# Performance work log

Measured on AMD Instinct MI355X. Metric: run time of the kernel, lower is better.

## Reference

```python
import jax, jax.numpy as jnp
import numpy as np

B, T, R, E, H = 64, 512, 256, 512, 1024

def setup_inputs() -> dict:
    key = jax.random.key(0)
    ks = jax.random.split(key, 7)
    s = lambda d: 1.0 / np.sqrt(d)
    return {
        "x": jax.random.normal(ks[0], (B, T, R), jnp.float32),
        "W_emb": jax.random.normal(ks[1], (E, R), jnp.float32) * s(R),
        "b_emb": jax.random.normal(ks[2], (E,), jnp.float32) * s(R),
        "W_ih": jax.random.normal(ks[3], (4 * H, E), jnp.float32) * s(H),
        "W_hh": jax.random.normal(ks[4], (4 * H, H), jnp.float32) * s(H),
        "b_ih": jax.random.normal(ks[5], (4 * H,), jnp.float32) * s(H),
        "b_hh": jax.random.normal(ks[6], (4 * H,), jnp.float32) * s(H),
    }

def reference(x, W_emb, b_emb, W_ih, W_hh, b_ih, b_hh):
    # Per-timestep Linear embedding, batched over time (same math as the loop)
    xe = jnp.einsum('btr,er->bte', x, W_emb) + b_emb            # [B,T,E]
    # Input contribution to all gates, precomputed for every step
    gx = jnp.einsum('bte,ge->btg', xe, W_ih) + (b_ih + b_hh)    # [B,T,4H]

    def step(carry, gx_t):
        h, c = carry
        gates = gx_t + h @ W_hh.T                               # [B,4H]
        i, f, g, o = jnp.split(gates, 4, axis=-1)
        i = jax.nn.sigmoid(i)
        f = jax.nn.sigmoid(f)
        g = jnp.tanh(g)
        o = jax.nn.sigmoid(o)
        c_new = f * c + i * g
        h_new = o * jnp.tanh(c_new)
        return (h_new, c_new), h_new

    h0 = jnp.zeros((x.shape[0], H), x.dtype)
    c0 = jnp.zeros((x.shape[0], H), x.dtype)
    (h_t, c_t), ys = jax.lax.scan(step, (h0, c0), jnp.swapaxes(gx, 0, 1))
    outputs = jnp.swapaxes(ys, 0, 1)                            # [B,T,H]
    return outputs, h_t, c_t
```

## Files before the change

### kernel.cpp

```cpp
#include <hip/hip_runtime.h>
#include <stdint.h>

typedef __attribute__((ext_vector_type(8))) short short8;
typedef __attribute__((ext_vector_type(4))) float f32x4;
typedef __attribute__((ext_vector_type(4))) unsigned short ushort4v;
typedef unsigned long long u64;

__device__ inline unsigned short f2bf(float x) {
  union { float f; unsigned u; } v; v.f = x;
  unsigned r = (v.u + 0x7FFFu + ((v.u >> 16) & 1u)) >> 16;
  return (unsigned short)r;
}
__device__ inline float bf2f(unsigned short b) {
  union { unsigned u; float f; } v; v.u = ((unsigned)b) << 16;
  return v.f;
}
__device__ inline float fsig(float x) { return 1.f / (1.f + __expf(-x)); }

__device__ inline void gload_lds16(const void* g, void* l) {
  __builtin_amdgcn_global_load_lds(
      (const __attribute__((address_space(1))) unsigned int*)g,
      (__attribute__((address_space(3))) unsigned int*)l, 16, 0, 0);
}

__global__ void k_convert(const float* __restrict__ src, unsigned short* __restrict__ dst, int n4) {
  int i = blockIdx.x * blockDim.x + threadIdx.x;
  if (i < n4) {
    f32x4 v = *(const f32x4*)(src + (size_t)i * 4);
    ushort4v r;
    r.x = f2bf(v.x); r.y = f2bf(v.y); r.z = f2bf(v.z); r.w = f2bf(v.w);
    *(ushort4v*)(dst + (size_t)i * 4) = r;
  }
}

__global__ void k_temb(const float* __restrict__ We, unsigned short* __restrict__ WT) {
  int o = blockIdx.x * blockDim.x + threadIdx.x;
  int r = o >> 9, e = o & 511;
  WT[o] = f2bf(We[e * 256 + r]);
}

__global__ void k_bcomb(const float* __restrict__ Wih, const float* __restrict__ b_emb,
                        const float* __restrict__ b_ih, const float* __restrict__ b_hh,
                        float* __restrict__ out) {
  int g = blockIdx.x * blockDim.x + threadIdx.x;
  const float* row = Wih + (size_t)g * 512;
  float s = 0.f;
  for (int e = 0; e < 512; ++e) s += row[e] * b_emb[e];
  out[g] = s + b_ih[g] + b_hh[g];
}

__global__ void k_init(unsigned short* __restrict__ h0, unsigned short* __restrict__ flags,
                       float* __restrict__ zerob) {
  int i = blockIdx.x * blockDim.x + threadIdx.x;
  h0[i] = 0;
  if (i < 256) { flags[i] = 0; zerob[i] = 0.f; }
}

template <int MODE>
__global__ __launch_bounds__(256) void k_gemm_bt(
    const unsigned short* __restrict__ A,
    const unsigned short* __restrict__ Bm,
    const float* __restrict__ bias,
    unsigned short* __restrict__ C,
    int M, int N, int K) {
  __shared__ unsigned short As[128 * 32];
  __shared__ unsigned short Bs[128 * 32];
  const int tid = threadIdx.x;

  int bidx = blockIdx.x, bidy = blockIdx.y;
  if (MODE == 1) {
    int bid = blockIdx.y * gridDim.x + blockIdx.x;
    int cpx = (gridDim.x * gridDim.y) >> 3;
    int swz = (bid & 7) * cpx + (bid >> 3);
    bidy = swz / gridDim.x;
    bidx = swz % gridDim.x;
  }
  const int m0 = bidy * 128, n0 = bidx * 128;
  const int lane = tid & 63, w = tid >> 6;
  const int wm = (w >> 1) * 64, wn = (w & 1) * 64;

  f32x4 acc[4][4] = {};

  const int ar0 = tid >> 2;
  const int ak = (tid & 3) * 8;
  const unsigned short* Ag0 = A + (size_t)(m0 + ar0) * K + ak;
  const unsigned short* Ag1 = A + (size_t)(m0 + 64 + ar0) * K + ak;
  const unsigned short* Bg0 = Bm + (size_t)(n0 + ar0) * K + ak;
  const unsigned short* Bg1 = Bm + (size_t)(n0 + 64 + ar0) * K + ak;
  unsigned short* Al = As + tid * 8;
  unsigned short* Bl = Bs + tid * 8;

  const int lr = lane & 15, lk = (lane >> 4) * 8;

  for (int k0 = 0; k0 < K; k0 += 32) {
    gload_lds16(Ag0 + k0, Al);
    gload_lds16(Ag1 + k0, Al + 2048);
    gload_lds16(Bg0 + k0, Bl);
    gload_lds16(Bg1 + k0, Bl + 2048);
    __syncthreads();
    short8 a[4], b[4];
#pragma unroll
    for (int i = 0; i < 4; i++) a[i] = *(const short8*)&As[(wm + i * 16 + lr) * 32 + lk];
#pragma unroll
    for (int j = 0; j < 4; j++) b[j] = *(const short8*)&Bs[(wn + j * 16 + lr) * 32 + lk];
#pragma unroll
    for (int i = 0; i < 4; i++)
#pragma unroll
      for (int j = 0; j < 4; j++)
        acc[i][j] = __builtin_amdgcn_mfma_f32_16x16x32_bf16(a[i], b[j], acc[i][j], 0, 0, 0);
    __syncthreads();
  }

  const int lq = (lane >> 4) * 4;
#pragma unroll
  for (int j = 0; j < 4; j++) {
    int col = n0 + wn + j * 16 + lr;
    float bv = bias[col];
#pragma unroll
    for (int i = 0; i < 4; i++) {
      int rowb = m0 + wm + i * 16 + lq;
#pragma unroll
      for (int r = 0; r < 4; r++) {
        int row = rowb + r;
        float v = acc[i][j][r] + bv;
        if (MODE == 1) {
          int t = row & 511, bglob = row >> 9;
          int gg = bglob >> 4, bb = bglob & 15;
          int s = col >> 10, cc = col & 1023;
          int gtb = cc >> 4, cl = cc & 15;
          int wv = cl >> 2, qq = cl & 3;
          size_t idx = (size_t)t * 262144 + (size_t)gg * 65536 + (size_t)gtb * 1024
                     + (size_t)((wv * 64 + bb * 4 + qq) * 4 + s);
          C[idx] = f2bf(v);
        } else {
          C[(size_t)row * (size_t)N + col] = f2bf(v);
        }
      }
    }
  }
}

#define R32(F) F(0) F(1) F(2) F(3) F(4) F(5) F(6) F(7) \
               F(8) F(9) F(10) F(11) F(12) F(13) F(14) F(15) \
               F(16) F(17) F(18) F(19) F(20) F(21) F(22) F(23) \
               F(24) F(25) F(26) F(27) F(28) F(29) F(30) F(31)
#define WDECL(i) short8 w##i;
#define WLOAD(i) asm volatile("global_load_dwordx4 %0, %1, off offset:%c2" \
                              : "=v"(w##i) : "v"(wbase), "i"((i) * 64));
#define MFH(i, ACC) { \
    short8 a_ = *(const short8*)(HsB + lB + (i) * 1024); \
    ACC = __builtin_amdgcn_mfma_f32_16x16x32_bf16(a_, w##i, ACC, 0, 0, 0); }
#define MF2(i, ACC) { \
    union { u64 d[2]; short8 s; } u_; \
    u_.d[0] = __hip_atomic_load((const u64*)(hrow2 + (i) * 32), __ATOMIC_RELAXED, __HIP_MEMORY_SCOPE_AGENT); \
    u_.d[1] = __hip_atomic_load((const u64*)(hrow2 + (i) * 32 + 4), __ATOMIC_RELAXED, __HIP_MEMORY_SCOPE_AGENT); \
    ACC = __builtin_amdgcn_mfma_f32_16x16x32_bf16(u_.s, w##i, ACC, 0, 0, 0); }

template <int RING>
__global__ __launch_bounds__(256, 1) void k_persist(
    const unsigned short* __restrict__ gx3,
    const unsigned short* __restrict__ Whh,
    unsigned short* __restrict__ hring,
    unsigned short* __restrict__ flags,
    float* __restrict__ out,
    float* __restrict__ hout,
    float* __restrict__ cout) {
  __shared__ unsigned short Hs[16384];
  __shared__ float Gs[4][16 * 17 + 4];

  const int tid = threadIdx.x;
  const int g = blockIdx.x & 3, gt = blockIdx.x >> 2;
  const int lane = tid & 63, w = tid >> 6;
  const int lr = lane & 15, hi = lane >> 4;

  const int grow = (lr >> 2) * 1024 + gt * 16 + w * 4 + (lr & 3);
  const unsigned short* wbase = Whh + (size_t)grow * 1024 + hi * 8;
  R32(WDECL)
  R32(WLOAD)
  asm volatile("s_waitcnt vmcnt(0)" ::: "memory");
  __builtin_amdgcn_sched_barrier(0);

  const int cb = lane >> 2, cq = lane & 3;
  const int col = gt * 16 + w * 4 + cq;
  const int brow = g * 16 + cb;
  float c_reg = 0.f;

  const u64* gbase = (const u64*)gx3 + (size_t)g * 16384 + (size_t)gt * 256;
  u64 gv = gbase[tid];

  const char* HsB = (const char*)Hs;
  const int lB = hi * 256 + lr * 16;

  const u64* fpw = (const u64*)flags + g * 16 + w * 4 + (lane & 3);

  for (int t = 0; t < 512; ++t) {
    f32x4 ac0 = {}, ac1 = {}, ac2 = {}, ac3 = {};
    if (RING == 2) {
      if (w == 0) {
        const u64* fp = (const u64*)flags + g * 16 + lane;
        for (;;) {
          bool ok = true;
          if (lane < 16) {
            u64 f = __hip_atomic_load(fp, __ATOMIC_RELAXED, __HIP_MEMORY_SCOPE_AGENT);
            ok = ((int)(f & 0xFFFF) >= t) && ((int)((f >> 16) & 0xFFFF) >= t) &&
                 ((int)((f >> 32) & 0xFFFF) >= t) && ((int)(f >> 48) >= t);
          }
          if (__all(ok)) break;
        }
      }
      __syncthreads();
      __builtin_amdgcn_sched_barrier(0);
      const unsigned short* hrow2 = hring + (size_t)(t & 1) * 65536
                                  + (size_t)(g * 16 + lr) * 1024 + hi * 8;
      MF2(0, ac0)  MF2(1, ac1)  MF2(2, ac2)  MF2(3, ac3)
      MF2(4, ac0)  MF2(5, ac1)  MF2(6, ac2)  MF2(7, ac3)
      MF2(8, ac0)  MF2(9, ac1)  MF2(10, ac2) MF2(11, ac3)
      MF2(12, ac0) MF2(13, ac1) MF2(14, ac2) MF2(15, ac3)
      MF2(16, ac0) MF2(17, ac1) MF2(18, ac2) MF2(19, ac3)
      MF2(20, ac0) MF2(21, ac1) MF2(22, ac2) MF2(23, ac3)
      MF2(24, ac0) MF2(25, ac1) MF2(26, ac2) MF2(27, ac3)
      MF2(28, ac0) MF2(29, ac1) MF2(30, ac2) MF2(31, ac3)
    } else {
      for (;;) {
        u64 f = __hip_atomic_load(fpw, __ATOMIC_RELAXED, __HIP_MEMORY_SCOPE_AGENT);
        bool ok = ((int)(f & 0xFFFF) >= t) && ((int)((f >> 16) & 0xFFFF) >= t) &&
                  ((int)((f >> 32) & 0xFFFF) >= t) && ((int)(f >> 48) >= t);
        if (__all(ok)) break;
      }
      __builtin_amdgcn_sched_barrier(0);
      const unsigned short* hsrc = hring + (size_t)t * 65536 + (size_t)g * 16384;
#pragma unroll
      for (int i = 0; i < 8; ++i) {
        int ch = w * 512 + i * 64;
        gload_lds16(hsrc + ((size_t)ch + lane) * 8, Hs + (size_t)ch * 8);
      }
      asm volatile("s_waitcnt vmcnt(0)" ::: "memory");
      __builtin_amdgcn_sched_barrier(0);
      __syncthreads();
      MFH(0, ac0)  MFH(1, ac1)  MFH(2, ac2)  MFH(3, ac3)
      MFH(4, ac0)  MFH(5, ac1)  MFH(6, ac2)  MFH(7, ac3)
      MFH(8, ac0)  MFH(9, ac1)  MFH(10, ac2) MFH(11, ac3)
      MFH(12, ac0) MFH(13, ac1) MFH(14, ac2) MFH(15, ac3)
      MFH(16, ac0) MFH(17, ac1) MFH(18, ac2) MFH(19, ac3)
      MFH(20, ac0) MFH(21, ac1) MFH(22, ac2) MFH(23, ac3)
      MFH(24, ac0) MFH(25, ac1) MFH(26, ac2) MFH(27, ac3)
      MFH(28, ac0) MFH(29, ac1) MFH(30, ac2) MFH(31, ac3)
    }
    f32x4 accs = (ac0 + ac1) + (ac2 + ac3);

#pragma unroll
    for (int r = 0; r < 4; ++r)
      Gs[w][(hi * 4 + r) * 17 + lr] = accs[r];
    asm volatile("s_waitcnt lgkmcnt(0)" ::: "memory");
    __builtin_amdgcn_sched_barrier(0);

    float gi = Gs[w][cb * 17 + 0 + cq]  + bf2f((unsigned short)(gv));
    float gf = Gs[w][cb * 17 + 4 + cq]  + bf2f((unsigned short)(gv >> 16));
    float gg = Gs[w][cb * 17 + 8 + cq]  + bf2f((unsigned short)(gv >> 32));
    float go = Gs[w][cb * 17 + 12 + cq] + bf2f((unsigned short)(gv >> 48));
    float i_ = fsig(gi);
    float f_ = fsig(gf);
    float g_ = tanhf(gg);
    float o_ = fsig(go);
    float cn = f_ * c_reg + i_ * g_;
    float hn = o_ * tanhf(cn);
    c_reg = cn;

    if (t == 511) {
      __builtin_nontemporal_store(hn, &out[((size_t)brow * 512 + t) * 1024 + col]);
      hout[(size_t)brow * 1024 + col] = hn;
      cout[(size_t)brow * 1024 + col] = cn;
    } else {
      unsigned hu = f2bf(hn);
      unsigned v0 = __shfl(hu, (lane & ~3) + 0);
      unsigned v1 = __shfl(hu, (lane & ~3) + 1);
      unsigned v2 = __shfl(hu, (lane & ~3) + 2);
      unsigned v3 = __shfl(hu, (lane & ~3) + 3);
      if ((lane & 3) == 0) {
        u64 pack = (u64)(v0 & 0xFFFF) | ((u64)(v1 & 0xFFFF) << 16)
                 | ((u64)(v2 & 0xFFFF) << 32) | ((u64)(v3 & 0xFFFF) << 48);
        u64* hp;
        if (RING == 2) {
          hp = (u64*)(hring + (size_t)((t + 1) & 1) * 65536
                      + (size_t)brow * 1024 + gt * 16 + w * 4);
        } else {
          size_t e = (size_t)(gt * 2 + (w >> 1)) * 128 + (size_t)cb * 8 + (size_t)(w & 1) * 4;
          hp = (u64*)(hring + (size_t)(t + 1) * 65536 + (size_t)g * 16384 + e);
        }
        __hip_atomic_store(hp, pack, __ATOMIC_RELAXED, __HIP_MEMORY_SCOPE_AGENT);
      }
      __syncthreads();
      if (tid == 0)
        __hip_atomic_store(&flags[g * 64 + gt], (unsigned short)(t + 1),
                           __ATOMIC_RELAXED, __HIP_MEMORY_SCOPE_AGENT);
      __builtin_nontemporal_store(hn, &out[((size_t)brow * 512 + t) * 1024 + col]);
      gv = gbase[(size_t)(t + 1) * 65536 + tid];
    }
  }
}
#undef MF2
#undef MFH
#undef WLOAD
#undef WDECL
#undef R32

extern "C" void kernel_launch(void* const* d_in, const int* in_sizes, int n_in,
                              void* d_out, int out_size, void* d_ws, size_t ws_size,
                              hipStream_t stream) {
  const float* x = (const float*)d_in[0];
  const float* W_emb = (const float*)d_in[1];
  const float* b_emb = (const float*)d_in[2];
  const float* W_ih = (const float*)d_in[3];
  const float* W_hh = (const float*)d_in[4];
  const float* b_ih = (const float*)d_in[5];
  const float* b_hh = (const float*)d_in[6];

  char* ws = (char*)d_ws;
  unsigned short* x_bf    = (unsigned short*)(ws + 0);
  unsigned short* WembT   = (unsigned short*)(ws + 16777216);
  unsigned short* Wih_bf  = (unsigned short*)(ws + 17039360);
  unsigned short* Whh_bf  = (unsigned short*)(ws + 21233664);
  float* b_comb           = (float*)(ws + 29622272);
  float* zerob            = (float*)(ws + 29638656);
  unsigned short* Wcomb   = (unsigned short*)(ws + 29639680);
  unsigned short* gx3     = (unsigned short*)(ws + 63193088);
  unsigned short* flags   = (unsigned short*)(ws + 331628544);
  unsigned short* hring   = (unsigned short*)(ws + 331632640);

  const size_t need_ring = 331632640ull + 512ull * 131072ull;
  const bool big = (ws_size >= need_ring);

  float* out = (float*)d_out;
  float* hout = out + (size_t)64 * 512 * 1024;
  float* cout = hout + 65536;

  k_convert<<<8192, 256, 0, stream>>>(x, x_bf, 2097152);
  k_convert<<<2048, 256, 0, stream>>>(W_ih, Wih_bf, 524288);
  k_convert<<<4096, 256, 0, stream>>>(W_hh, Whh_bf, 1048576);
  k_temb<<<512, 256, 0, stream>>>(W_emb, WembT);
  k_bcomb<<<16, 256, 0, stream>>>(W_ih, b_emb, b_ih, b_hh, b_comb);
  k_init<<<256, 256, 0, stream>>>(hring, flags, zerob);

  k_gemm_bt<0><<<dim3(2, 32), 256, 0, stream>>>(Wih_bf, WembT, zerob, Wcomb, 4096, 256, 512);
  k_gemm_bt<1><<<dim3(32, 256), 256, 0, stream>>>(x_bf, Wcomb, b_comb, gx3, 32768, 4096, 256);

  if (big)
    k_persist<512><<<256, 256, 0, stream>>>(gx3, Whh_bf, hring, flags, out, hout, cout);
  else
    k_persist<2><<<256, 256, 0, stream>>>(gx3, Whh_bf, hring, flags, out, hout, cout);
}
```

Measured before the change: 2.052 ms.

## Reorder x rows time-major and split gx into per-gate planes

The x conversion now writes rows in time-major order (t*64+b), so the input-projection GEMM epilogue writes contiguous rows for each timestep. The gx buffer moves from interleaved 4-gate u64 packs to four separate gate planes, which makes the GEMM's scattered 2-byte stores more coalesced. The persistent recurrent kernel now does four 2-byte loads per step from separate planes where it used to do one 8-byte load. This trades faster GEMM output writes for more, smaller loads inside the serial time loop.

```diff
diff --git a/kernel.cpp b/kernel.cpp
--- a/kernel.cpp
+++ b/kernel.cpp
@@ -22,6 +22,8 @@
       (const __attribute__((address_space(1))) unsigned int*)g,
       (__attribute__((address_space(3))) unsigned int*)l, 16, 0, 0);
 }
+
+#define GXPLANE 33554432ull
 
 __global__ void k_convert(const float* __restrict__ src, unsigned short* __restrict__ dst, int n4) {
   int i = blockIdx.x * blockDim.x + threadIdx.x;
@@ -31,6 +33,16 @@
     r.x = f2bf(v.x); r.y = f2bf(v.y); r.z = f2bf(v.z); r.w = f2bf(v.w);
     *(ushort4v*)(dst + (size_t)i * 4) = r;
   }
+}
+
+__global__ void k_convert_x(const float* __restrict__ src, unsigned short* __restrict__ dst) {
+  int i = blockIdx.x * blockDim.x + threadIdx.x;
+  int p = i * 4;
+  int b = p >> 17, rem = p & 131071, t = rem >> 8, k = rem & 255;
+  f32x4 v = *(const f32x4*)(src + (size_t)p);
+  ushort4v r;
+  r.x = f2bf(v.x); r.y = f2bf(v.y); r.z = f2bf(v.z); r.w = f2bf(v.w);
+  *(ushort4v*)(dst + ((size_t)(t * 64 + b) << 8) + k) = r;
 }
 
 __global__ void k_temb(const float* __restrict__ We, unsigned short* __restrict__ WT) {
@@ -124,13 +136,14 @@
         int row = rowb + r;
         float v = acc[i][j][r] + bv;
         if (MODE == 1) {
-          int t = row & 511, bglob = row >> 9;
+          int t = row >> 6, bglob = row & 63;
           int gg = bglob >> 4, bb = bglob & 15;
           int s = col >> 10, cc = col & 1023;
           int gtb = cc >> 4, cl = cc & 15;
           int wv = cl >> 2, qq = cl & 3;
-          size_t idx = (size_t)t * 262144 + (size_t)gg * 65536 + (size_t)gtb * 1024
-                     + (size_t)((wv * 64 + bb * 4 + qq) * 4 + s);
+          size_t idx = (size_t)s * GXPLANE
+                     + ((size_t)t * 64 + (size_t)gtb) * 1024
+                     + (size_t)gg * 256 + (size_t)(wv * 64 + bb * 4 + qq);
           C[idx] = f2bf(v);
         } else {
           C[(size_t)row * (size_t)N + col] = f2bf(v);
@@ -185,8 +198,8 @@
   const int brow = g * 16 + cb;
   float c_reg = 0.f;
 
-  const u64* gbase = (const u64*)gx3 + (size_t)g * 16384 + (size_t)gt * 256;
-  u64 gv = gbase[tid];
+  const unsigned short* gp0 = gx3 + (size_t)gt * 1024 + (size_t)g * 256 + tid;
+  unsigned short gv0 = gp0[0], gv1 = gp0[GXPLANE], gv2 = gp0[2 * GXPLANE], gv3 = gp0[3 * GXPLANE];
 
   const char* HsB = (const char*)Hs;
   const int lB = hi * 256 + lr * 16;
@@ -254,10 +267,10 @@
     asm volatile("s_waitcnt lgkmcnt(0)" ::: "memory");
     __builtin_amdgcn_sched_barrier(0);
 
-    float gi = Gs[w][cb * 17 + 0 + cq]  + bf2f((unsigned short)(gv));
-    float gf = Gs[w][cb * 17 + 4 + cq]  + bf2f((unsigned short)(gv >> 16));
-    float gg = Gs[w][cb * 17 + 8 + cq]  + bf2f((unsigned short)(gv >> 32));
-    float go = Gs[w][cb * 17 + 12 + cq] + bf2f((unsigned short)(gv >> 48));
+    float gi = Gs[w][cb * 17 + 0 + cq]  + bf2f(gv0);
+    float gf = Gs[w][cb * 17 + 4 + cq]  + bf2f(gv1);
+    float gg = Gs[w][cb * 17 + 8 + cq]  + bf2f(gv2);
+    float go = Gs[w][cb * 17 + 12 + cq] + bf2f(gv3);
     float i_ = fsig(gi);
     float f_ = fsig(gf);
     float g_ = tanhf(gg);
@@ -294,7 +307,9 @@
         __hip_atomic_store(&flags[g * 64 + gt], (unsigned short)(t + 1),
                            __ATOMIC_RELAXED, __HIP_MEMORY_SCOPE_AGENT);
       __builtin_nontemporal_store(hn, &out[((size_t)brow * 512 + t) * 1024 + col]);
-      gv = gbase[(size_t)(t + 1) * 65536 + tid];
+      const unsigned short* gp = gx3 + (size_t)(t + 1) * 65536 + (size_t)gt * 1024
+                               + (size_t)g * 256 + tid;
+      gv0 = gp[0]; gv1 = gp[GXPLANE]; gv2 = gp[2 * GXPLANE]; gv3 = gp[3 * GXPLANE];
     }
   }
 }
@@ -334,7 +349,7 @@
   float* hout = out + (size_t)64 * 512 * 1024;
   float* cout = hout + 65536;
 
-  k_convert<<<8192, 256, 0, stream>>>(x, x_bf, 2097152);
+  k_convert_x<<<8192, 256, 0, stream>>>(x, x_bf);
   k_convert<<<2048, 256, 0, stream>>>(W_ih, Wih_bf, 524288);
   k_convert<<<4096, 256, 0, stream>>>(W_hh, Whh_bf, 1048576);
   k_temb<<<512, 256, 0, stream>>>(W_emb, WembT);
```

Measured after the change: 1.806 ms. 1.14x faster.
